# Performance work log

Hardware: AMD Instinct MI355X
Metric: run time of the kernel (lower is better)

The kernel has to match this reference:

```python
import jax, jax.numpy as jnp
import numpy as np

B, S, D_IN, D_OUT, H = 2, 2048, 1024, 1024, 16
HD = D_OUT // H


def setup_inputs() -> dict:
    key = jax.random.key(0)
    ks = jax.random.split(key, 6)
    x = jax.random.normal(ks[0], (B, S, D_IN), jnp.float32)
    Wq = jax.random.normal(ks[1], (D_IN, D_OUT), jnp.float32) * 0.02
    Wk = jax.random.normal(ks[2], (D_IN, D_OUT), jnp.float32) * 0.02
    Wv = jax.random.normal(ks[3], (D_IN, D_OUT), jnp.float32) * 0.02
    Wo = jax.random.normal(ks[4], (D_OUT, D_OUT), jnp.float32) * 0.02
    bo = jax.random.normal(ks[5], (D_OUT,), jnp.float32) * 0.02
    return {"x": x, "Wq": Wq, "Wk": Wk, "Wv": Wv, "Wo": Wo, "bo": bo}


def reference(x, Wq, Wk, Wv, Wo, bo):
    b, s, _ = x.shape

    def to_heads(t):  # [b, s, d_out] -> [b, h, s, hd]
        return t.reshape(b, s, H, HD).transpose(0, 2, 1, 3)

    Q = to_heads(x @ Wq)
    K = to_heads(x @ Wk)
    V = to_heads(x @ Wv)

    scale = 1.0 / jnp.sqrt(jnp.asarray(HD, x.dtype))
    scores = jnp.einsum("bhqd,bhkd->bhqk", Q, K) * scale
    causal_mask = jnp.triu(jnp.ones((s, s), dtype=bool), k=1)  # True above diag
    scores = jnp.where(causal_mask, jnp.asarray(-1e6, scores.dtype), scores)
    weights = jax.nn.softmax(scores, axis=-1)  # dropout p=0.0 -> identity
    attn = jnp.einsum("bhqk,bhkd->bhqd", weights, V)  # [b, h, s, hd]
    # Faithful to source: reshape [b,h,s,hd] -> [b,s,d_out] WITHOUT head transpose-back
    attn = attn.reshape(b, s, D_OUT)
    return attn @ Wo + bo
```

## Files before the change

### kernel.cpp

```cpp
#include <hip/hip_runtime.h>
#include <stdint.h>


typedef unsigned short u16;
typedef __attribute__((ext_vector_type(8))) short bf16x8;
typedef __attribute__((ext_vector_type(4))) float f32x4;

#define MFMA_BF16(a, b, c) __builtin_amdgcn_mfma_f32_16x16x32_bf16((a), (b), (c), 0, 0, 0)
#define QSCALE 0.18033688011112042f

__device__ __forceinline__ u16 f2bf(float f) {
  union { float f; unsigned int u; } x; x.f = f;
  unsigned int r = x.u + 0x7fffu + ((x.u >> 16) & 1u);
  return (u16)(r >> 16);
}
__device__ __forceinline__ bf16x8 pack8(float4 a, float4 b) {
  bf16x8 r;
  r[0] = (short)f2bf(a.x); r[1] = (short)f2bf(a.y);
  r[2] = (short)f2bf(a.z); r[3] = (short)f2bf(a.w);
  r[4] = (short)f2bf(b.x); r[5] = (short)f2bf(b.y);
  r[6] = (short)f2bf(b.z); r[7] = (short)f2bf(b.w);
  return r;
}
__device__ __forceinline__ void gload_lds16(const u16* g, u16* l) {
  __builtin_amdgcn_global_load_lds((__attribute__((address_space(1))) void*)g,
                                   (__attribute__((address_space(3))) void*)l, 16, 0, 0);
}

template <int CPR>
__device__ __forceinline__ int sw_off(int r, int c) {
  return (r * CPR + (c ^ (r & (CPR - 1)))) * 8;
}

__global__ __launch_bounds__(1024) void prep(
    const float* __restrict__ x, u16* __restrict__ xb,
    const float* __restrict__ Wq, const float* __restrict__ Wk,
    const float* __restrict__ Wv, const float* __restrict__ Wo,
    u16* __restrict__ WoT, u16* __restrict__ WT3) {
  const int bxg = blockIdx.x, by = blockIdx.y;
  if (bxg >= 128) {
    const int blk = (bxg - 128) * 32 + by;
    const int tid = threadIdx.y * 32 + threadIdx.x;
    const size_t i = ((size_t)blk * 1024 + tid) * 8;
    const float4 a = *(const float4*)&x[i];
    const float4 b2 = *(const float4*)&x[i + 4];
    *(bf16x8*)&xb[i] = pack8(a, b2);
    return;
  }
  __shared__ u16 t[32][33];
  const float* W;
  u16* T;
  int j0, wcol;
  if (bxg < 32) {
    j0 = bxg * 32; wcol = j0; W = Wo; T = WoT;
  } else {
    j0 = (bxg - 32) * 32;
    const int g = j0 >> 10;
    W = (g == 0) ? Wq : (g == 1) ? Wk : Wv;
    T = WT3;
    wcol = j0 & 1023;
  }
  const int k0 = by * 32;
  t[threadIdx.y][threadIdx.x] =
      f2bf(W[(size_t)(k0 + threadIdx.y) * 1024 + wcol + threadIdx.x]);
  __syncthreads();
  T[(size_t)(j0 + threadIdx.y) * 1024 + k0 + threadIdx.x] = t[threadIdx.x][threadIdx.y];
}

__global__ __launch_bounds__(256) void x_to_bf16(const float* __restrict__ x,
                                                 u16* __restrict__ xb) {
  const size_t i = ((size_t)blockIdx.x * 256 + threadIdx.x) * 8;
  const float4 a = *(const float4*)&x[i];
  const float4 b = *(const float4*)&x[i + 4];
  *(bf16x8*)&xb[i] = pack8(a, b);
}

__global__ void transpose_cols(const float* __restrict__ W0, const float* __restrict__ W1,
                               const float* __restrict__ W2, u16* __restrict__ T,
                               int h0, int hsx64) {
  __shared__ u16 t[32][33];
  const int j0 = blockIdx.x * 32;
  const int g = j0 / hsx64;
  const float* W = (g == 0) ? W0 : (g == 1) ? W1 : W2;
  const int wc0 = h0 * 64 + (j0 % hsx64);
  const int k0 = blockIdx.y * 32;
  t[threadIdx.y][threadIdx.x] =
      f2bf(W[(size_t)(k0 + threadIdx.y) * 1024 + wc0 + threadIdx.x]);
  __syncthreads();
  T[(size_t)(j0 + threadIdx.y) * 1024 + k0 + threadIdx.x] = t[threadIdx.x][threadIdx.y];
}

template <int MODE, int AF32>
__global__ __launch_bounds__(256, 2) void gemm_bt(
    const void* __restrict__ Av, const u16* __restrict__ BT,
    void* __restrict__ C0v, u16* __restrict__ C1, u16* __restrict__ C2,
    const float* __restrict__ bias, int M, int N, int K, int hs, int h0) {
  __shared__ __align__(16) u16 lsA[128 * 32];
  __shared__ __align__(16) u16 lsB[128 * 32];
  const int tid = threadIdx.x, lane = tid & 63, wv = tid >> 6;
  const int quad = lane >> 4, l16 = lane & 15;
  const int m0 = blockIdx.y * 128, n0 = blockIdx.x * 128;
  const int wm = (wv >> 1) * 64, wn = (wv & 1) * 64;
  const int hs64 = hs * 64;
  f32x4 acc[4][4] = {};

  for (int k0 = 0; k0 < K; k0 += 32) {
    if constexpr (AF32) {
      bf16x8 va[2], vb[2];
#pragma unroll
      for (int c = 0; c < 2; ++c) {
        const int P = c * 256 + tid, r = P >> 2, cc = P & 3;
        const float* Af = (const float*)Av;
        const float4 a0 = *(const float4*)&Af[(size_t)(m0 + r) * K + k0 + cc * 8];
        const float4 a1 = *(const float4*)&Af[(size_t)(m0 + r) * K + k0 + cc * 8 + 4];
        va[c] = pack8(a0, a1);
        vb[c] = *(const bf16x8*)&BT[(size_t)(n0 + r) * K + k0 + cc * 8];
      }
      __syncthreads();
#pragma unroll
      for (int c = 0; c < 2; ++c) {
        const int P = c * 256 + tid, r = P >> 2, cc = P & 3;
        *(bf16x8*)&lsA[sw_off<4>(r, cc)] = va[c];
        *(bf16x8*)&lsB[sw_off<4>(r, cc)] = vb[c];
      }
      __syncthreads();
    } else {
      __syncthreads();
#pragma unroll
      for (int c = 0; c < 2; ++c) {
        const int P = c * 256 + tid, r = P >> 2;
        const int gcol = ((P & 3) ^ (r & 3)) * 8;
        gload_lds16((const u16*)Av + (size_t)(m0 + r) * K + k0 + gcol,
                    &lsA[(size_t)(c * 256 + wv * 64) * 8]);
        gload_lds16(BT + (size_t)(n0 + r) * K + k0 + gcol,
                    &lsB[(size_t)(c * 256 + wv * 64) * 8]);
      }
      __syncthreads();
    }
    bf16x8 af[4], bfr[4];
#pragma unroll
    for (int i = 0; i < 4; ++i) af[i] = *(const bf16x8*)&lsA[sw_off<4>(wm + i * 16 + l16, quad)];
#pragma unroll
    for (int j = 0; j < 4; ++j) bfr[j] = *(const bf16x8*)&lsB[sw_off<4>(wn + j * 16 + l16, quad)];
#pragma unroll
    for (int i = 0; i < 4; ++i)
#pragma unroll
      for (int j = 0; j < 4; ++j) acc[i][j] = MFMA_BF16(af[i], bfr[j], acc[i][j]);
  }

#pragma unroll
  for (int i = 0; i < 4; ++i)
#pragma unroll
    for (int j = 0; j < 4; ++j) {
      const int n = n0 + wn + j * 16 + l16;
      float bv = 0.f;
      if constexpr (MODE == 1) bv = bias[n];
#pragma unroll
      for (int r = 0; r < 4; ++r) {
        const int m = m0 + wm + i * 16 + quad * 4 + r;
        if constexpr (MODE == 3) {
          const int b = m >> 11, s = m & 2047;
          if (n < hs64) {
            ((u16*)C0v)[((size_t)b * 2048 + s) * hs64 + n] = f2bf(acc[i][j][r] * QSCALE);
          } else if (n < 2 * hs64) {
            C1[((size_t)b * 2048 + s) * hs64 + (n - hs64)] = f2bf(acc[i][j][r]);
          } else {
            const int nn = n - 2 * hs64;
            C2[((size_t)(b * hs + (nn >> 6)) * 64 + (nn & 63)) * 2048 + s] =
                f2bf(acc[i][j][r]);
          }
        } else {
          const int b = (m >= hs * 128) ? 1 : 0;
          const int rp = m - b * hs * 128;
          ((float*)C0v)[(size_t)(b * 2048 + h0 * 128 + rp) * 1024 + n] =
              acc[i][j][r] + bv;
        }
      }
    }
}

__global__ __launch_bounds__(256, 2) void attn_fwd(
    const u16* __restrict__ Qsl, const u16* __restrict__ Ksl,
    const u16* __restrict__ VTsl, u16* __restrict__ A2sl, int hs) {
  __shared__ __align__(16) u16 lsK[2][64 * 64];
  __shared__ __align__(16) u16 lsV[2][64 * 64];
  __shared__ __align__(16) u16 lsP[4][16 * 64];
  __shared__ __align__(16) float scrl[64];
  const int tid = threadIdx.x, lane = tid & 63, wv = tid >> 6;
  const int quad = lane >> 4, l16 = lane & 15;
  const int grp = wv >> 1, wq = wv & 1;

  const int cpx = gridDim.x >> 3;
  const int w = (blockIdx.x & 7) * cpx + (blockIdx.x >> 3);
  const int bh = w >> 4, bx = w & 15;

  const int b = (bh >= hs) ? 1 : 0, hh = bh - b * hs;
  const int hs64 = hs * 64;
  const u16* Qb = Qsl + (size_t)b * 2048 * hs64;
  const u16* Kb = Ksl + (size_t)b * 2048 * hs64;
  const u16* Vb = VTsl + (size_t)(b * hs + hh) * 64 * 2048;
  u16* A2b = A2sl + (size_t)(b * hs + hh) * 2048 * 64;
  u16* lsPw = &lsP[wv][0];
  float* scro = (float*)&lsK[0][0];

  bf16x8 ones;
#pragma unroll
  for (int i = 0; i < 8; ++i) ones[i] = (short)0x3F80;

  const int prow = l16 >> 1;
  const int pb0 = (l16 & 1) << 2;

  const int Pa = tid, ra = Pa >> 3, ca = (Pa & 7) ^ (ra & 7);
  const int Pb2 = 256 + tid, rb = Pb2 >> 3, cb = (Pb2 & 7) ^ (rb & 7);
  const size_t kTileStep = (size_t)64 * hs64;
  const u16* const kBa = Kb + (size_t)ra * hs64 + hh * 64 + ca * 8;
  const u16* const kBb = Kb + (size_t)rb * hs64 + hh * 64 + cb * 8;
  const u16* const vBa = Vb + (size_t)ra * 2048 + ca * 8;
  const u16* const vBb = Vb + (size_t)rb * 2048 + cb * 8;
  const int dA = (wv * 64) * 8;
  const int dB = (256 + wv * 64) * 8;

  for (int half = 0; half < 2; ++half) {
    const int qt = (half == 0) ? bx : 31 - bx;
    const int q0 = qt * 64;

    bf16x8 qf[2][2];
#pragma unroll
    for (int j = 0; j < 2; ++j)
#pragma unroll
      for (int ks = 0; ks < 2; ++ks)
        qf[j][ks] = *(const bf16x8*)&Qb[(size_t)(q0 + wq * 32 + j * 16 + l16) * hs64 +
                                        hh * 64 + ks * 32 + quad * 8];

    f32x4 acc_o[2][4] = {};
    f32x4 acc_l[2] = {};

    const u16* pkA = kBa;
    const u16* pkB = kBb;
    const u16* pvA = vBa;
    const u16* pvB = vBb;

    __syncthreads();
    gload_lds16(pkA, &lsK[0][dA]);
    gload_lds16(pkB, &lsK[0][dB]);
    gload_lds16(pvA, &lsV[0][dA]);
    gload_lds16(pvB, &lsV[0][dB]);

    auto body = [&](int buf, bool domask) {
      f32x4 accs[2][2] = {};
#pragma unroll
      for (int ks = 0; ks < 2; ++ks)
#pragma unroll
        for (int nj = 0; nj < 2; ++nj) {
          const bf16x8 kf = *(const bf16x8*)
              &lsK[buf][sw_off<8>(grp * 32 + nj * 16 + l16, ks * 4 + quad)];
          accs[0][nj] = MFMA_BF16(kf, qf[0][ks], accs[0][nj]);
          accs[1][nj] = MFMA_BF16(kf, qf[1][ks], accs[1][nj]);
        }
#pragma unroll
      for (int j = 0; j < 2; ++j) {
        const int grow = wq * 32 + j * 16 + l16;
#pragma unroll
        for (int nj = 0; nj < 2; ++nj) {
#pragma unroll
          for (int r = 0; r < 4; ++r) {
            float p = exp2f(accs[j][nj][r]);
            if (domask) {
              const int keyb = grp * 32 + nj * 16 + quad * 4;
              p = (keyb + r > grow) ? 0.f : p;
            }
            accs[j][nj][r] = p;
          }
          union { float f; unsigned int u; } t0, t1, t2, t3;
          t0.f = accs[j][nj][0]; t1.f = accs[j][nj][1];
          t2.f = accs[j][nj][2]; t3.f = accs[j][nj][3];
          uint2 wpk;
          wpk.x = (t0.u >> 16) | (t1.u & 0xFFFF0000u);
          wpk.y = (t2.u >> 16) | (t3.u & 0xFFFF0000u);
          const int row = j * 8 + prow;
          const int chunk = (pb0 + 2 * nj + (quad >> 1)) ^ prow;
          *(uint2*)&lsPw[row * 64 + chunk * 8 + (quad & 1) * 4] = wpk;
        }
      }
      bf16x8 pf[2];
#pragma unroll
      for (int j = 0; j < 2; ++j) {
        const int row = j * 8 + prow;
        const int chunk = (pb0 + quad) ^ prow;
        pf[j] = *(const bf16x8*)&lsPw[row * 64 + chunk * 8];
        acc_l[j] = MFMA_BF16(ones, pf[j], acc_l[j]);
      }
#pragma unroll
      for (int njo = 0; njo < 4; ++njo) {
        const bf16x8 vf = *(const bf16x8*)
            &lsV[buf][sw_off<8>(njo * 16 + l16, grp * 4 + quad)];
        acc_o[0][njo] = MFMA_BF16(vf, pf[0], acc_o[0][njo]);
        acc_o[1][njo] = MFMA_BF16(vf, pf[1], acc_o[1][njo]);
      }
    };

    for (int kt = 0; kt < qt; ++kt) {
      const int buf = kt & 1, nb = buf ^ 1;
      __syncthreads();
      pkA += kTileStep; pkB += kTileStep; pvA += 64; pvB += 64;
      gload_lds16(pkA, &lsK[nb][dA]);
      gload_lds16(pkB, &lsK[nb][dB]);
      gload_lds16(pvA, &lsV[nb][dA]);
      gload_lds16(pvB, &lsV[nb][dB]);
      body(buf, false);
    }
    {
      __syncthreads();
      body(qt & 1, true);
    }

    __syncthreads();
    if (grp == 1) {
#pragma unroll
      for (int j = 0; j < 2; ++j) {
#pragma unroll
        for (int njo = 0; njo < 4; ++njo) {
          const int ch = (njo * 4 + quad) ^ l16;
          *(f32x4*)&scro[(size_t)(wq * 32 + j * 16 + l16) * 64 + ch * 4] =
              acc_o[j][njo];
        }
        if (quad == 0) scrl[wq * 32 + j * 16 + l16] = acc_l[j][0];
      }
    }
    __syncthreads();
    if (grp == 0) {
#pragma unroll
      for (int j = 0; j < 2; ++j) {
        const int ql = wq * 32 + j * 16 + l16;
        const float inv = 1.0f / (acc_l[j][0] + scrl[ql]);
#pragma unroll
        for (int njo = 0; njo < 4; ++njo) {
          const int ch = (njo * 4 + quad) ^ l16;
          const f32x4 ob = *(const f32x4*)&scro[(size_t)ql * 64 + ch * 4];
          uint2 o;
          o.x = (unsigned)f2bf((acc_o[j][njo][0] + ob[0]) * inv) |
                ((unsigned)f2bf((acc_o[j][njo][1] + ob[1]) * inv) << 16);
          o.y = (unsigned)f2bf((acc_o[j][njo][2] + ob[2]) * inv) |
                ((unsigned)f2bf((acc_o[j][njo][3] + ob[3]) * inv) << 16);
          *(uint2*)&A2b[(size_t)(q0 + ql) * 64 + njo * 16 + quad * 4] = o;
        }
      }
    }
  }
}

extern "C" void kernel_launch(void* const* d_in, const int* in_sizes, int n_in,
                              void* d_out, int out_size, void* d_ws, size_t ws_size,
                              hipStream_t stream) {
  (void)in_sizes; (void)n_in; (void)out_size;
  const float* x  = (const float*)d_in[0];
  const float* Wq = (const float*)d_in[1];
  const float* Wk = (const float*)d_in[2];
  const float* Wv = (const float*)d_in[3];
  const float* Wo = (const float*)d_in[4];
  const float* bo = (const float*)d_in[5];
  float* out = (float*)d_out;
  char* ws = (char*)d_ws;
  const size_t MB = 1024 * 1024;
  const size_t KB = 1024;

  int hs = 2;
  if      (ws_size >= 2 * MB + 16 * 2432 * KB) hs = 16;
  else if (ws_size >= 2 * MB +  8 * 2432 * KB) hs = 8;
  else if (ws_size >= 2 * MB +  4 * 2432 * KB) hs = 4;

  u16* WoT   = (u16*)(ws);
  u16* Ksl   = (u16*)(ws + 2 * MB);
  u16* VTsl  = (u16*)(ws + 2 * MB + (size_t)hs *  512 * KB);
  u16* A2sl  = (u16*)(ws + 2 * MB + (size_t)hs * 1024 * KB);
  u16* WT3sl = (u16*)(ws + 2 * MB + (size_t)hs * 1536 * KB);
  u16* Qsl   = (u16*)(ws + 2 * MB + (size_t)hs * 1920 * KB);

  if (hs == 16) {
    u16* xb = A2sl;
    prep<<<dim3(144, 32), dim3(32, 32), 0, stream>>>(x, xb, Wq, Wk, Wv, Wo, WoT, WT3sl);
    gemm_bt<3, 0><<<dim3(24, 32), 256, 0, stream>>>(
        (const void*)xb, WT3sl, (void*)Qsl, Ksl, VTsl, nullptr, 4096, 3072, 1024, 16, 0);
    attn_fwd<<<dim3(512), 256, 0, stream>>>(Qsl, Ksl, VTsl, A2sl, 16);
    gemm_bt<1, 0><<<dim3(8, 32), 256, 0, stream>>>(
        (const void*)A2sl, WoT, (void*)out, nullptr, nullptr, bo, 4096, 1024, 1024, 16, 0);
  } else {
    transpose_cols<<<dim3(32, 32), dim3(32, 32), 0, stream>>>(Wo, Wo, Wo, WoT, 0, 1024);
    for (int h0 = 0; h0 < 16; h0 += hs) {
      transpose_cols<<<dim3(6 * hs, 32), dim3(32, 32), 0, stream>>>(Wq, Wk, Wv, WT3sl, h0, hs * 64);
      gemm_bt<3, 1><<<dim3((3 * hs) / 2, 32), 256, 0, stream>>>(
          (const void*)x, WT3sl, (void*)Qsl, Ksl, VTsl, nullptr, 4096, 3 * hs * 64, 1024, hs, h0);
      attn_fwd<<<dim3(16 * 2 * hs), 256, 0, stream>>>(Qsl, Ksl, VTsl, A2sl, hs);
      gemm_bt<1, 0><<<dim3(8, 2 * hs), 256, 0, stream>>>(
          (const void*)A2sl, WoT, (void*)out, nullptr, nullptr, bo, 2 * hs * 128, 1024, 1024, hs, h0);
    }
  }
}
```

Baseline: 191.8 us.

## Double-buffer LDS tiles in bf16 GEMM and vectorize transposed V stores

The bf16-input GEMM path now uses two LDS buffers, issuing global-to-LDS loads for the next K tile while MFMAs run on the current one, with one barrier per iteration instead of two. The QKV projection epilogue also packs four consecutive bf16 values into one 8-byte store when writing the transposed V output. The aim is to hide global load latency and cut the number of narrow scattered stores. The cost is doubled LDS use per block, which could lower occupancy.

```diff
diff --git a/kernel.cpp b/kernel.cpp
--- a/kernel.cpp
+++ b/kernel.cpp
@@ -95,8 +95,8 @@
     const void* __restrict__ Av, const u16* __restrict__ BT,
     void* __restrict__ C0v, u16* __restrict__ C1, u16* __restrict__ C2,
     const float* __restrict__ bias, int M, int N, int K, int hs, int h0) {
-  __shared__ __align__(16) u16 lsA[128 * 32];
-  __shared__ __align__(16) u16 lsB[128 * 32];
+  __shared__ __align__(16) u16 lsA[2][128 * 32];
+  __shared__ __align__(16) u16 lsB[2][128 * 32];
   const int tid = threadIdx.x, lane = tid & 63, wv = tid >> 6;
   const int quad = lane >> 4, l16 = lane & 15;
   const int m0 = blockIdx.y * 128, n0 = blockIdx.x * 128;
@@ -104,8 +104,47 @@
   const int hs64 = hs * 64;
   f32x4 acc[4][4] = {};
 
-  for (int k0 = 0; k0 < K; k0 += 32) {
-    if constexpr (AF32) {
+  if constexpr (!AF32) {
+#pragma unroll
+    for (int c = 0; c < 2; ++c) {
+      const int P = c * 256 + tid, r = P >> 2;
+      const int gcol = ((P & 3) ^ (r & 3)) * 8;
+      gload_lds16((const u16*)Av + (size_t)(m0 + r) * K + gcol,
+                  &lsA[0][(c * 256 + wv * 64) * 8]);
+      gload_lds16(BT + (size_t)(n0 + r) * K + gcol,
+                  &lsB[0][(c * 256 + wv * 64) * 8]);
+    }
+    __syncthreads();
+    const int nk = K >> 5;
+    for (int kt = 0; kt < nk; ++kt) {
+      const int buf = kt & 1;
+      if (kt + 1 < nk) {
+        const int k1 = (kt + 1) << 5;
+#pragma unroll
+        for (int c = 0; c < 2; ++c) {
+          const int P = c * 256 + tid, r = P >> 2;
+          const int gcol = ((P & 3) ^ (r & 3)) * 8;
+          gload_lds16((const u16*)Av + (size_t)(m0 + r) * K + k1 + gcol,
+                      &lsA[buf ^ 1][(c * 256 + wv * 64) * 8]);
+          gload_lds16(BT + (size_t)(n0 + r) * K + k1 + gcol,
+                      &lsB[buf ^ 1][(c * 256 + wv * 64) * 8]);
+        }
+      }
+      bf16x8 af[4], bfr[4];
+#pragma unroll
+      for (int i = 0; i < 4; ++i)
+        af[i] = *(const bf16x8*)&lsA[buf][sw_off<4>(wm + i * 16 + l16, quad)];
+#pragma unroll
+      for (int j = 0; j < 4; ++j)
+        bfr[j] = *(const bf16x8*)&lsB[buf][sw_off<4>(wn + j * 16 + l16, quad)];
+#pragma unroll
+      for (int i = 0; i < 4; ++i)
+#pragma unroll
+        for (int j = 0; j < 4; ++j) acc[i][j] = MFMA_BF16(af[i], bfr[j], acc[i][j]);
+      __syncthreads();
+    }
+  } else {
+    for (int k0 = 0; k0 < K; k0 += 32) {
       bf16x8 va[2], vb[2];
 #pragma unroll
       for (int c = 0; c < 2; ++c) {
@@ -120,63 +159,68 @@
 #pragma unroll
       for (int c = 0; c < 2; ++c) {
         const int P = c * 256 + tid, r = P >> 2, cc = P & 3;
-        *(bf16x8*)&lsA[sw_off<4>(r, cc)] = va[c];
-        *(bf16x8*)&lsB[sw_off<4>(r, cc)] = vb[c];
+        *(bf16x8*)&lsA[0][sw_off<4>(r, cc)] = va[c];
+        *(bf16x8*)&lsB[0][sw_off<4>(r, cc)] = vb[c];
       }
       __syncthreads();
-    } else {
-      __syncthreads();
-#pragma unroll
-      for (int c = 0; c < 2; ++c) {
-        const int P = c * 256 + tid, r = P >> 2;
-        const int gcol = ((P & 3) ^ (r & 3)) * 8;
-        gload_lds16((const u16*)Av + (size_t)(m0 + r) * K + k0 + gcol,
-                    &lsA[(size_t)(c * 256 + wv * 64) * 8]);
-        gload_lds16(BT + (size_t)(n0 + r) * K + k0 + gcol,
-                    &lsB[(size_t)(c * 256 + wv * 64) * 8]);
-      }
-      __syncthreads();
-    }
-    bf16x8 af[4], bfr[4];
-#pragma unroll
-    for (int i = 0; i < 4; ++i) af[i] = *(const bf16x8*)&lsA[sw_off<4>(wm + i * 16 + l16, quad)];
-#pragma unroll
-    for (int j = 0; j < 4; ++j) bfr[j] = *(const bf16x8*)&lsB[sw_off<4>(wn + j * 16 + l16, quad)];
-#pragma unroll
-    for (int i = 0; i < 4; ++i)
-#pragma unroll
-      for (int j = 0; j < 4; ++j) acc[i][j] = MFMA_BF16(af[i], bfr[j], acc[i][j]);
-  }
-
-#pragma unroll
-  for (int i = 0; i < 4; ++i)
+      bf16x8 af[4], bfr[4];
+#pragma unroll
+      for (int i = 0; i < 4; ++i)
+        af[i] = *(const bf16x8*)&lsA[0][sw_off<4>(wm + i * 16 + l16, quad)];
+#pragma unroll
+      for (int j = 0; j < 4; ++j)
+        bfr[j] = *(const bf16x8*)&lsB[0][sw_off<4>(wn + j * 16 + l16, quad)];
+#pragma unroll
+      for (int i = 0; i < 4; ++i)
+#pragma unroll
+        for (int j = 0; j < 4; ++j) acc[i][j] = MFMA_BF16(af[i], bfr[j], acc[i][j]);
+    }
+  }
+
+  if constexpr (MODE == 3) {
 #pragma unroll
     for (int j = 0; j < 4; ++j) {
       const int n = n0 + wn + j * 16 + l16;
-      float bv = 0.f;
-      if constexpr (MODE == 1) bv = bias[n];
-#pragma unroll
-      for (int r = 0; r < 4; ++r) {
-        const int m = m0 + wm + i * 16 + quad * 4 + r;
-        if constexpr (MODE == 3) {
-          const int b = m >> 11, s = m & 2047;
-          if (n < hs64) {
-            ((u16*)C0v)[((size_t)b * 2048 + s) * hs64 + n] = f2bf(acc[i][j][r] * QSCALE);
-          } else if (n < 2 * hs64) {
-            C1[((size_t)b * 2048 + s) * hs64 + (n - hs64)] = f2bf(acc[i][j][r]);
-          } else {
-            const int nn = n - 2 * hs64;
-            C2[((size_t)(b * hs + (nn >> 6)) * 64 + (nn & 63)) * 2048 + s] =
-                f2bf(acc[i][j][r]);
-          }
+#pragma unroll
+      for (int i = 0; i < 4; ++i) {
+        const int mb = m0 + wm + i * 16 + quad * 4;
+        const int b = mb >> 11, s0 = mb & 2047;
+        if (n < hs64) {
+#pragma unroll
+          for (int r = 0; r < 4; ++r)
+            ((u16*)C0v)[((size_t)b * 2048 + s0 + r) * hs64 + n] =
+                f2bf(acc[i][j][r] * QSCALE);
+        } else if (n < 2 * hs64) {
+#pragma unroll
+          for (int r = 0; r < 4; ++r)
+            C1[((size_t)b * 2048 + s0 + r) * hs64 + (n - hs64)] = f2bf(acc[i][j][r]);
         } else {
+          const int nn = n - 2 * hs64;
+          uint2 o;
+          o.x = (unsigned)f2bf(acc[i][j][0]) | ((unsigned)f2bf(acc[i][j][1]) << 16);
+          o.y = (unsigned)f2bf(acc[i][j][2]) | ((unsigned)f2bf(acc[i][j][3]) << 16);
+          *(uint2*)&C2[((size_t)(b * hs + (nn >> 6)) * 64 + (nn & 63)) * 2048 + s0] = o;
+        }
+      }
+    }
+  } else {
+#pragma unroll
+    for (int i = 0; i < 4; ++i)
+#pragma unroll
+      for (int j = 0; j < 4; ++j) {
+        const int n = n0 + wn + j * 16 + l16;
+        float bv = 0.f;
+        if constexpr (MODE == 1) bv = bias[n];
+#pragma unroll
+        for (int r = 0; r < 4; ++r) {
+          const int m = m0 + wm + i * 16 + quad * 4 + r;
           const int b = (m >= hs * 128) ? 1 : 0;
           const int rp = m - b * hs * 128;
           ((float*)C0v)[(size_t)(b * 2048 + h0 * 128 + rp) * 1024 + n] =
               acc[i][j][r] + bv;
         }
       }
-    }
+  }
 }
 
 __global__ __launch_bounds__(256, 2) void attn_fwd(
```

Measured after the change: 185.2 us. -3.4%, faster.
